# Kernel optimization log

Measured on AMD Instinct MI355X. Metric: run time of the kernel, lower is better.

## Reference

```python
import jax, jax.numpy as jnp
import numpy as np

D_MODEL = 1024
N_HEADS = 16
D_K = D_MODEL // N_HEADS  # 64
N_CLASSES = 32
S_LEN = 16   # synonyms per class
BATCH = 32
T_LEN = 512  # key/value sequence length


def setup_inputs() -> dict:
    key = jax.random.key(0)
    k1, k2, k3, k4, k5, k6 = jax.random.split(key, 6)
    Q = jax.random.normal(k1, (N_CLASSES, S_LEN, D_MODEL), dtype=jnp.float32)
    H = jax.random.normal(k2, (BATCH, T_LEN, D_MODEL), dtype=jnp.float32)
    ql = jax.random.normal(k3, (N_CLASSES, D_MODEL), dtype=jnp.float32)
    # torch Linear weights are (out_features, in_features), init N(0, 0.001)
    WQ_w = 0.001 * jax.random.normal(k4, (D_MODEL, D_MODEL), dtype=jnp.float32)
    WK_w = 0.001 * jax.random.normal(k5, (D_MODEL, D_MODEL), dtype=jnp.float32)
    WV_w = 0.001 * jax.random.normal(k6, (D_MODEL, D_MODEL), dtype=jnp.float32)
    return {"Q": Q, "H": H, "ql": ql, "WQ_w": WQ_w, "WK_w": WK_w, "WV_w": WV_w}


def reference(Q, H, ql, WQ_w, WK_w, WV_w):
    c, s, d = Q.shape
    b, t, _ = H.shape
    nh, dk = N_HEADS, D_K
    # projections (torch Linear: x @ W.T)
    q_s = (Q @ WQ_w.T).reshape(c, s, nh, dk).transpose(0, 2, 1, 3)   # czsh
    k_s = (H @ WK_w.T).reshape(b, t, nh, dk).transpose(0, 2, 1, 3)   # bzth
    Wql = ql @ WV_w.T                                                # ch
    Hh = H.reshape(b, t, nh, dk).transpose(0, 2, 1, 3)               # bzth
    WK = jnp.tanh(k_s)
    K = jnp.tanh(Hh)
    # scores: (b, c, z, s, t)
    scores = jnp.einsum('bzth,czsh->bczst', WK, q_s)
    attn = jax.nn.softmax(scores, axis=-1)
    # context: (b, c, z, s, h)
    context = jnp.einsum('bzth,bczst->bczsh', K, attn)
    # AvgPool3d((1, s, 1)) + squeeze(-2): mean over s -> (b, c, z, h)
    ctx = context.mean(axis=3).reshape(b, c, nh * dk)                # (b, c, d_model)
    output = jnp.einsum('bch,ch->bc', ctx, Wql)
    return output
```

## Files before the change

### kernel.cpp

```cpp
#include <hip/hip_runtime.h>
#include <hip/hip_bf16.h>
#include <math.h>

#define D_MODEL 1024
#define N_HEADS 16
#define D_K 64
#define N_CLASSES 32
#define S_LEN 16
#define BATCH 32
#define T_LEN 512

typedef __bf16 bf16_t;
typedef bf16_t bf16x8 __attribute__((ext_vector_type(8)));
typedef float f32x4 __attribute__((ext_vector_type(4)));
typedef long lx2 __attribute__((ext_vector_type(2)));

__device__ inline unsigned short f2bf(float f) {
    unsigned int u = __float_as_uint(f);
    unsigned int r = (u + 0x7FFFu + ((u >> 16) & 1u)) >> 16;
    return (unsigned short)r;
}
__device__ inline float fast_tanh(float x) {
    float e = __expf(2.0f * x);
    return (e - 1.0f) * __builtin_amdgcn_rcpf(e + 1.0f);
}
__device__ inline float4 fast_tanh4(float4 v) {
    return make_float4(fast_tanh(v.x), fast_tanh(v.y), fast_tanh(v.z), fast_tanh(v.w));
}
__device__ inline float dot4(float4 a, float4 b) {
    return a.x * b.x + a.y * b.y + a.z * b.z + a.w * b.w;
}
__device__ inline int pack_fp8x4(float4 v) {
    int p = __builtin_amdgcn_cvt_pk_fp8_f32(v.x, v.y, 0, false);
    p = __builtin_amdgcn_cvt_pk_fp8_f32(v.z, v.w, p, true);
    return p;
}

__device__ inline void async16(void* lds, const void* g) {
    __builtin_amdgcn_global_load_lds(
        (const __attribute__((address_space(1))) unsigned int*)g,
        (__attribute__((address_space(3))) unsigned int*)lds, 16, 0, 0);
}

__global__ __launch_bounds__(256) void cvt2_fp8_sw(
    const float* __restrict__ inA, int* __restrict__ outA, int nA,
    const float* __restrict__ inB, int* __restrict__ outB, int nB, float sB)
{
    int i = blockIdx.x * 256 + threadIdx.x;
    const float* in;
    int* out;
    float s;
    if (i < nA) { in = inA; out = outA; s = 1.0f; }
    else {
        i -= nA;
        if (i >= nB) return;
        in = inB; out = outB; s = sB;
    }
    const int p = i << 2;
    const int blk = p >> 10;
    const int pos = p & 1023;
    const int rb = blk >> 4;
    const int kb = blk & 15;
    const int q = pos >> 4;
    const int quad = q >> 4, l16 = q & 15;
    const int o = pos & 15;
    const int kh = o >> 3, b0 = o & 7;
    const int r = rb * 16 + l16;
    const int k = kb * 64 + kh * 32 + quad * 8 + b0;
    float4 v = *(const float4*)(in + (size_t)r * 1024 + k);
    v.x *= s; v.y *= s; v.z *= s; v.w *= s;
    out[i] = pack_fp8x4(v);
}

__global__ __launch_bounds__(256) void cvt2_bf16(
    const float4* __restrict__ inA, ushort4* __restrict__ outA, int nA4,
    const float4* __restrict__ inB, ushort4* __restrict__ outB, int nB4)
{
    int i = blockIdx.x * 256 + threadIdx.x;
    const float4* in;
    ushort4* out;
    if (i < nA4) { in = inA + i; out = outA + i; }
    else {
        i -= nA4;
        if (i >= nB4) return;
        in = inB + i; out = outB + i;
    }
    float4 v = *in;
    ushort4 o;
    o.x = f2bf(v.x); o.y = f2bf(v.y); o.z = f2bf(v.z); o.w = f2bf(v.w);
    *out = o;
}

__global__ __launch_bounds__(256) void cvt_bf16(
    const float4* __restrict__ in, ushort4* __restrict__ out, int n4)
{
    int i = blockIdx.x * 256 + threadIdx.x;
    if (i < n4) {
        float4 v = in[i];
        ushort4 o;
        o.x = f2bf(v.x); o.y = f2bf(v.y); o.z = f2bf(v.z); o.w = f2bf(v.w);
        out[i] = o;
    }
}

__global__ __launch_bounds__(256) void gemm_fp8_bt(
    const unsigned char* __restrict__ A, const unsigned char* __restrict__ B,
    unsigned short* __restrict__ C, int M, int N, float outScale)
{
    __shared__ __align__(16) unsigned char As[8192];
    __shared__ __align__(16) unsigned char Bs[8192];
    const int tid = threadIdx.x;
    const int m0 = blockIdx.x * 128;
    const int n0 = blockIdx.y * 128;
    const int wid = tid >> 6;
    const int lane = tid & 63;
    const int quad = lane >> 4;
    const int l16 = lane & 15;
    const int wm = (wid >> 1) * 64;
    const int wn = (wid & 1) * 64;
    const int stA = wm >> 4;
    const int stB = wn >> 4;
    const int st = tid >> 6;
    const int cl = (tid & 63) * 16;

    f32x4 acc[4][4] = {};

    const unsigned char* Ab = A + ((size_t)(m0 >> 4) * 16) * 1024;
    const unsigned char* Bb = B + ((size_t)(n0 >> 4) * 16) * 1024;

    for (int kb = 0; kb < 16; kb++) {
        async16(&As[tid * 16],        Ab + ((size_t)st * 16 + kb) * 1024 + cl);
        async16(&As[4096 + tid * 16], Ab + ((size_t)(st + 4) * 16 + kb) * 1024 + cl);
        async16(&Bs[tid * 16],        Bb + ((size_t)st * 16 + kb) * 1024 + cl);
        async16(&Bs[4096 + tid * 16], Bb + ((size_t)(st + 4) * 16 + kb) * 1024 + cl);
        __syncthreads();

        lx2 a8[4], b8[4];
#pragma unroll
        for (int mt = 0; mt < 4; mt++)
            a8[mt] = *(const lx2*)&As[(stA + mt) * 1024 + lane * 16];
#pragma unroll
        for (int nt = 0; nt < 4; nt++)
            b8[nt] = *(const lx2*)&Bs[(stB + nt) * 1024 + lane * 16];
#pragma unroll
        for (int mt = 0; mt < 4; mt++)
#pragma unroll
            for (int nt = 0; nt < 4; nt++) {
                acc[mt][nt] = __builtin_amdgcn_mfma_f32_16x16x32_fp8_fp8(
                    a8[mt].x, b8[nt].x, acc[mt][nt], 0, 0, 0);
                acc[mt][nt] = __builtin_amdgcn_mfma_f32_16x16x32_fp8_fp8(
                    a8[mt].y, b8[nt].y, acc[mt][nt], 0, 0, 0);
            }
        __syncthreads();
    }

#pragma unroll
    for (int mt = 0; mt < 4; mt++)
#pragma unroll
        for (int nt = 0; nt < 4; nt++)
#pragma unroll
            for (int r = 0; r < 4; r++) {
                const int row = m0 + wm + mt * 16 + quad * 4 + r;
                const int col = n0 + wn + nt * 16 + l16;
                C[(size_t)row * N + col] = f2bf(fast_tanh(acc[mt][nt][r] * outScale));
            }
}

__global__ __launch_bounds__(256) void gemm_bf16_bt(
    const unsigned short* __restrict__ A, const unsigned short* __restrict__ B,
    unsigned short* __restrict__ C, int M, int N, int K)
{
    __shared__ unsigned short As[128 * 32];
    __shared__ unsigned short Bs[128 * 32];
    const int tid = threadIdx.x;
    const int m0 = blockIdx.x * 128;
    const int n0 = blockIdx.y * 128;
    const int wid = tid >> 6;
    const int lane = tid & 63;
    const int quad = lane >> 4;
    const int l16 = lane & 15;
    const int wm = (wid >> 1) * 64;
    const int wn = (wid & 1) * 64;

    f32x4 acc[4][4] = {};

    const int r0 = tid >> 2;
    const int cc0 = (tid & 3) * 8;

    for (int k0 = 0; k0 < K; k0 += 32) {
        async16(&As[tid * 8],        A + (size_t)(m0 + r0) * K + k0 + cc0);
        async16(&As[2048 + tid * 8], A + (size_t)(m0 + 64 + r0) * K + k0 + cc0);
        async16(&Bs[tid * 8],        B + (size_t)(n0 + r0) * K + k0 + cc0);
        async16(&Bs[2048 + tid * 8], B + (size_t)(n0 + 64 + r0) * K + k0 + cc0);
        __syncthreads();

        bf16x8 af[4], bfr[4];
#pragma unroll
        for (int mt = 0; mt < 4; mt++)
            af[mt] = *(const bf16x8*)&As[(wm + mt * 16 + l16) * 32 + quad * 8];
#pragma unroll
        for (int nt = 0; nt < 4; nt++)
            bfr[nt] = *(const bf16x8*)&Bs[(wn + nt * 16 + l16) * 32 + quad * 8];
#pragma unroll
        for (int mt = 0; mt < 4; mt++)
#pragma unroll
            for (int nt = 0; nt < 4; nt++)
                acc[mt][nt] = __builtin_amdgcn_mfma_f32_16x16x32_bf16(
                    af[mt], bfr[nt], acc[mt][nt], 0, 0, 0);
        __syncthreads();
    }

#pragma unroll
    for (int mt = 0; mt < 4; mt++)
#pragma unroll
        for (int nt = 0; nt < 4; nt++)
#pragma unroll
            for (int r = 0; r < 4; r++) {
                const int row = m0 + wm + mt * 16 + quad * 4 + r;
                const int col = n0 + wn + nt * 16 + l16;
                C[(size_t)row * N + col] = f2bf(acc[mt][nt][r]);
            }
}

__global__ __launch_bounds__(256) void wql_kernel(
    const float* __restrict__ ql, const float* __restrict__ WV, float* __restrict__ wql)
{
    __shared__ float4 qls[32][32];
    __shared__ float4 WVs[64][33];
    const int tid = threadIdx.x;
    const int n0 = blockIdx.x * 64;
    const int k0 = blockIdx.y * 128;

    for (int i = tid; i < 1024; i += 256)
        qls[i >> 5][i & 31] = *(const float4*)(ql + (size_t)(i >> 5) * D_MODEL + k0 + (i & 31) * 4);
    for (int i = tid; i < 2048; i += 256)
        WVs[i >> 5][i & 31] = *(const float4*)(WV + (size_t)(n0 + (i >> 5)) * D_MODEL + k0 + (i & 31) * 4);
    __syncthreads();

    const int n = tid & 63;
    const int c0 = (tid >> 6) * 8;
    float acc[8] = {};
    for (int kq = 0; kq < 32; kq++) {
        const float4 wv = WVs[n][kq];
#pragma unroll
        for (int c = 0; c < 8; c++) acc[c] += dot4(qls[c0 + c][kq], wv);
    }
#pragma unroll
    for (int c = 0; c < 8; c++)
        atomicAdd(&wql[(size_t)(c0 + c) * D_MODEL + n0 + n], acc[c]);
}

__global__ __launch_bounds__(256) void kv_gemm(
    const float* __restrict__ H, const unsigned short* __restrict__ wql16,
    float* __restrict__ kv)
{
    __shared__ unsigned short Ks[128 * 64];
    __shared__ float kvt[128 * 33];
    const int chunk = blockIdx.x;
    const int z = blockIdx.y;
    const int b = chunk >> 2;
    const int t0 = (chunk & 3) * 128;
    const int tid = threadIdx.x;
    const int wid = tid >> 6;
    const int lane = tid & 63;
    const int quad = lane >> 4;
    const int l16 = lane & 15;

#pragma unroll
    for (int it = 0; it < 8; it++) {
        const int idx = it * 256 + tid;
        const int row = idx >> 4;
        const int c4 = (idx & 15) * 4;
        float4 v = *(const float4*)(H + ((size_t)b * T_LEN + t0 + row) * D_MODEL + z * D_K + c4);
        v = fast_tanh4(v);
        ushort4 o;
        o.x = f2bf(v.x); o.y = f2bf(v.y); o.z = f2bf(v.z); o.w = f2bf(v.w);
        *(ushort4*)&Ks[row * 64 + c4] = o;
    }
    bf16x8 bfr[2][2];
#pragma unroll
    for (int ct = 0; ct < 2; ct++)
#pragma unroll
        for (int kh = 0; kh < 2; kh++)
            bfr[ct][kh] = *(const bf16x8*)(wql16 +
                (size_t)(ct * 16 + l16) * D_MODEL + z * D_K + kh * 32 + quad * 8);
    __syncthreads();

    const int wt = wid * 32;
    f32x4 acc[2][2] = {};
#pragma unroll
    for (int tt = 0; tt < 2; tt++) {
        const bf16x8 a0 = *(const bf16x8*)&Ks[(wt + tt * 16 + l16) * 64 + quad * 8];
        const bf16x8 a1 = *(const bf16x8*)&Ks[(wt + tt * 16 + l16) * 64 + 32 + quad * 8];
#pragma unroll
        for (int ct = 0; ct < 2; ct++) {
            acc[tt][ct] = __builtin_amdgcn_mfma_f32_16x16x32_bf16(a0, bfr[ct][0], acc[tt][ct], 0, 0, 0);
            acc[tt][ct] = __builtin_amdgcn_mfma_f32_16x16x32_bf16(a1, bfr[ct][1], acc[tt][ct], 0, 0, 0);
        }
    }
#pragma unroll
    for (int tt = 0; tt < 2; tt++)
#pragma unroll
        for (int ct = 0; ct < 2; ct++)
#pragma unroll
            for (int r = 0; r < 4; r++)
                kvt[(wt + tt * 16 + quad * 4 + r) * 33 + ct * 16 + l16] = acc[tt][ct][r];
    __syncthreads();

    float* outb = kv + (((size_t)b * 16 + z) * 32) * 512 + t0;
#pragma unroll
    for (int it = 0; it < 4; it++) {
        const int idx = it * 256 + tid;
        const int c = idx >> 5;
        const int tq = (idx & 31) * 4;
        float4 v = make_float4(kvt[(tq + 0) * 33 + c], kvt[(tq + 1) * 33 + c],
                               kvt[(tq + 2) * 33 + c], kvt[(tq + 3) * 33 + c]);
        *(float4*)(outb + (size_t)c * 512 + tq) = v;
    }
}

__global__ __launch_bounds__(512, 4) void attn_mfma(
    const unsigned short* __restrict__ qproj, const unsigned short* __restrict__ wkt,
    const float* __restrict__ kv, float* __restrict__ out)
{
    __shared__ unsigned short wkts[512 * 64];
    const int z = blockIdx.x;
    const int b = blockIdx.y;
    const int tid = threadIdx.x;
    const int wid = tid >> 6;
    const int lane = tid & 63;
    const int quad = lane >> 4;
    const int l16 = lane & 15;

    const unsigned short* wb = wkt + (size_t)(b * T_LEN) * D_MODEL + z * D_K;
#pragma unroll
    for (int it = 0; it < 8; it++) {
        const int chunk = it * 512 + tid;
        const int row = chunk >> 3;
        const int c = chunk & 7;
        async16(&wkts[chunk * 8], wb + (size_t)row * D_MODEL + ((c ^ (row & 7)) * 8));
    }

    bf16x8 af[4][2];
#pragma unroll
    for (int ct = 0; ct < 4; ct++)
#pragma unroll
        for (int kh = 0; kh < 2; kh++)
            af[ct][kh] = *(const bf16x8*)(qproj +
                (size_t)((wid * 4 + ct) * 16 + l16) * D_MODEL + z * D_K + kh * 32 + quad * 8);
    __syncthreads();

    float den[4][4], num[4][4];
#pragma unroll
    for (int ct = 0; ct < 4; ct++)
#pragma unroll
        for (int r = 0; r < 4; r++) { den[ct][r] = 0.f; num[ct][r] = 0.f; }

    const float* kvb = kv + (((size_t)b * 16 + z) * 32) * 512;
    const int x0 = (quad ^ (l16 & 7)) * 8;
    const int x1 = ((quad ^ 4) ^ (l16 & 7)) * 8;
    for (int nt = 0; nt < 32; nt++) {
        const int rbase = (nt * 16 + l16) * 64;
        const bf16x8 b0 = *(const bf16x8*)&wkts[rbase + x0];
        const bf16x8 b1 = *(const bf16x8*)&wkts[rbase + x1];
#pragma unroll
        for (int ct = 0; ct < 4; ct++) {
            f32x4 a = {};
            a = __builtin_amdgcn_mfma_f32_16x16x32_bf16(af[ct][0], b0, a, 0, 0, 0);
            a = __builtin_amdgcn_mfma_f32_16x16x32_bf16(af[ct][1], b1, a, 0, 0, 0);
            const float kvv = kvb[(size_t)(wid * 4 + ct) * 512 + nt * 16 + l16];
#pragma unroll
            for (int r = 0; r < 4; r++) {
                const float e = __expf(a[r]);
                den[ct][r] += e;
                num[ct][r] += e * kvv;
            }
        }
    }

#pragma unroll
    for (int ct = 0; ct < 4; ct++) {
        float s = 0.f;
#pragma unroll
        for (int r = 0; r < 4; r++) {
            float d = den[ct][r], n = num[ct][r];
#pragma unroll
            for (int off = 1; off < 16; off <<= 1) {
                d += __shfl_xor(d, off, 64);
                n += __shfl_xor(n, off, 64);
            }
            s += n / d;
        }
        s += __shfl_xor(s, 16, 64);
        s += __shfl_xor(s, 32, 64);
        if (lane == 0)
            atomicAdd(&out[b * N_CLASSES + wid * 4 + ct], s * (1.0f / 16.0f));
    }
}

extern "C" void kernel_launch(void* const* d_in, const int* in_sizes, int n_in,
                              void* d_out, int out_size, void* d_ws, size_t ws_size,
                              hipStream_t stream)
{
    const float* Q  = (const float*)d_in[0];
    const float* H  = (const float*)d_in[1];
    const float* ql = (const float*)d_in[2];
    const float* WQ = (const float*)d_in[3];
    const float* WK = (const float*)d_in[4];
    const float* WV = (const float*)d_in[5];
    float* out = (float*)d_out;

    char* ws = (char*)d_ws;
    unsigned char*  Hf8   = (unsigned char*)(ws);
    unsigned short* wkt_b = (unsigned short*)(ws + (size_t)33554432);
    float*          kv    = (float*)(ws + (size_t)67108864);
    unsigned char*  WKf8  = (unsigned char*)(ws + (size_t)100663296);
    unsigned short* Qb      = (unsigned short*)(ws);
    unsigned short* WQb     = (unsigned short*)(ws + (size_t)(1 << 20));
    unsigned short* qproj_b = (unsigned short*)(ws + (size_t)(3 << 20));
    float*          wqlb    = (float*)(ws + (size_t)(4 << 20));
    unsigned short* wqlb16  = (unsigned short*)(ws + (size_t)4718592);

    hipMemsetAsync(d_out, 0, (size_t)out_size * sizeof(float), stream);

    dim3 thr(256);
    cvt2_fp8_sw<<<dim3(17408), thr, 0, stream>>>(
        H, (int*)Hf8, 4194304,
        WK, (int*)WKf8, 262144, 512.0f);
    gemm_fp8_bt<<<dim3(128, 8), thr, 0, stream>>>(Hf8, WKf8, wkt_b, 16384, 1024, 1.0f / 512.0f);
    cvt2_bf16<<<dim3(1536), thr, 0, stream>>>(
        (const float4*)Q, (ushort4*)Qb, 131072,
        (const float4*)WQ, (ushort4*)WQb, 262144);
    gemm_bf16_bt<<<dim3(4, 8), thr, 0, stream>>>(Qb, WQb, qproj_b, 512, 1024, 1024);
    hipMemsetAsync(wqlb, 0, (size_t)N_CLASSES * D_MODEL * sizeof(float), stream);
    wql_kernel<<<dim3(16, 8), thr, 0, stream>>>(ql, WV, wqlb);
    cvt_bf16<<<dim3(32), thr, 0, stream>>>((const float4*)wqlb, (ushort4*)wqlb16, 8192);
    kv_gemm<<<dim3(128, 16), thr, 0, stream>>>(H, wqlb16, kv);
    attn_mfma<<<dim3(16, 32), dim3(512), 0, stream>>>(qproj_b, wkt_b, kv, out);
}
```

Measured before the change: 239.8 us.

## Merge prep and GEMM kernels into fused launches, prefetch kv in attention

Collapses the eight prep and GEMM launches plus two memsets into two kernels that dispatch by block index: one for all conversions and the ql·WV projection, one for the fp8 WK GEMM, the bf16 Q GEMM and the kv GEMM. The wql projection now does the full K loop per block and writes bf16 directly, so the fp32 atomics and the memset go away. The attention kernel prefetches the next kv values one iteration ahead and raises wave priority around the MFMAs. Its final atomicAdd becomes per-head partial writes that a small reduce kernel sums. The aim is to cut launch gaps, serialization and atomics, at the cost of an extra launch and a wql path that no longer uses shared memory.

```diff
diff --git a/kernel.cpp b/kernel.cpp
--- a/kernel.cpp
+++ b/kernel.cpp
@@ -42,286 +42,244 @@
         (__attribute__((address_space(3))) unsigned int*)lds, 16, 0, 0);
 }
 
-__global__ __launch_bounds__(256) void cvt2_fp8_sw(
-    const float* __restrict__ inA, int* __restrict__ outA, int nA,
-    const float* __restrict__ inB, int* __restrict__ outB, int nB, float sB)
+__global__ __launch_bounds__(256) void prep_kernel(
+    const float* __restrict__ H, int* __restrict__ Hf8,
+    const float* __restrict__ WK, int* __restrict__ WKf8,
+    const float4* __restrict__ Q, ushort4* __restrict__ Qb,
+    const float4* __restrict__ WQ, ushort4* __restrict__ WQb,
+    const float* __restrict__ ql, const float* __restrict__ WV,
+    unsigned short* __restrict__ wqlb16)
 {
-    int i = blockIdx.x * 256 + threadIdx.x;
-    const float* in;
-    int* out;
-    float s;
-    if (i < nA) { in = inA; out = outA; s = 1.0f; }
-    else {
-        i -= nA;
-        if (i >= nB) return;
-        in = inB; out = outB; s = sB;
-    }
-    const int p = i << 2;
-    const int blk = p >> 10;
-    const int pos = p & 1023;
-    const int rb = blk >> 4;
-    const int kb = blk & 15;
-    const int q = pos >> 4;
-    const int quad = q >> 4, l16 = q & 15;
-    const int o = pos & 15;
-    const int kh = o >> 3, b0 = o & 7;
-    const int r = rb * 16 + l16;
-    const int k = kb * 64 + kh * 32 + quad * 8 + b0;
-    float4 v = *(const float4*)(in + (size_t)r * 1024 + k);
-    v.x *= s; v.y *= s; v.z *= s; v.w *= s;
-    out[i] = pack_fp8x4(v);
-}
-
-__global__ __launch_bounds__(256) void cvt2_bf16(
-    const float4* __restrict__ inA, ushort4* __restrict__ outA, int nA4,
-    const float4* __restrict__ inB, ushort4* __restrict__ outB, int nB4)
-{
-    int i = blockIdx.x * 256 + threadIdx.x;
-    const float4* in;
-    ushort4* out;
-    if (i < nA4) { in = inA + i; out = outA + i; }
-    else {
-        i -= nA4;
-        if (i >= nB4) return;
-        in = inB + i; out = outB + i;
-    }
-    float4 v = *in;
-    ushort4 o;
-    o.x = f2bf(v.x); o.y = f2bf(v.y); o.z = f2bf(v.z); o.w = f2bf(v.w);
-    *out = o;
-}
-
-__global__ __launch_bounds__(256) void cvt_bf16(
-    const float4* __restrict__ in, ushort4* __restrict__ out, int n4)
-{
-    int i = blockIdx.x * 256 + threadIdx.x;
-    if (i < n4) {
-        float4 v = in[i];
+    const int bid = blockIdx.x;
+    const int tid = threadIdx.x;
+    if (bid < 16) {
+        const int n0 = bid * 64;
+        const int n = tid & 63;
+        const int c0 = (tid >> 6) * 8;
+        const float* wvp = WV + (size_t)(n0 + n) * D_MODEL;
+        float acc[8] = {};
+        for (int k = 0; k < 1024; k += 4) {
+            const float4 wv = *(const float4*)(wvp + k);
+#pragma unroll
+            for (int c = 0; c < 8; c++) {
+                const float4 qv = *(const float4*)(ql + (size_t)(c0 + c) * D_MODEL + k);
+                acc[c] += dot4(qv, wv);
+            }
+        }
+#pragma unroll
+        for (int c = 0; c < 8; c++)
+            wqlb16[(size_t)(c0 + c) * D_MODEL + n0 + n] = f2bf(acc[c]);
+    } else if (bid < 17424) {
+        int i = (bid - 16) * 256 + tid;
+        const float* in; int* out; float s;
+        if (i < 4194304) { in = H; out = Hf8; s = 1.0f; }
+        else { i -= 4194304; in = WK; out = WKf8; s = 512.0f; }
+        const int p = i << 2;
+        const int blk = p >> 10;
+        const int pos = p & 1023;
+        const int rb = blk >> 4, kb = blk & 15;
+        const int q = pos >> 4;
+        const int quad = q >> 4, l16 = q & 15;
+        const int o = pos & 15;
+        const int kh = o >> 3, b0 = o & 7;
+        const int r = rb * 16 + l16;
+        const int k = kb * 64 + kh * 32 + quad * 8 + b0;
+        float4 v = *(const float4*)(in + (size_t)r * 1024 + k);
+        v.x *= s; v.y *= s; v.z *= s; v.w *= s;
+        out[i] = pack_fp8x4(v);
+    } else {
+        int i = (bid - 17424) * 256 + tid;
+        const float4* in; ushort4* out;
+        if (i < 131072) { in = Q + i; out = Qb + i; }
+        else { i -= 131072; in = WQ + i; out = WQb + i; }
+        float4 v = *in;
         ushort4 o;
         o.x = f2bf(v.x); o.y = f2bf(v.y); o.z = f2bf(v.z); o.w = f2bf(v.w);
-        out[i] = o;
+        *out = o;
     }
 }
 
-__global__ __launch_bounds__(256) void gemm_fp8_bt(
-    const unsigned char* __restrict__ A, const unsigned char* __restrict__ B,
-    unsigned short* __restrict__ C, int M, int N, float outScale)
-{
-    __shared__ __align__(16) unsigned char As[8192];
-    __shared__ __align__(16) unsigned char Bs[8192];
-    const int tid = threadIdx.x;
-    const int m0 = blockIdx.x * 128;
-    const int n0 = blockIdx.y * 128;
-    const int wid = tid >> 6;
-    const int lane = tid & 63;
-    const int quad = lane >> 4;
-    const int l16 = lane & 15;
-    const int wm = (wid >> 1) * 64;
-    const int wn = (wid & 1) * 64;
-    const int stA = wm >> 4;
-    const int stB = wn >> 4;
-    const int st = tid >> 6;
-    const int cl = (tid & 63) * 16;
-
-    f32x4 acc[4][4] = {};
-
-    const unsigned char* Ab = A + ((size_t)(m0 >> 4) * 16) * 1024;
-    const unsigned char* Bb = B + ((size_t)(n0 >> 4) * 16) * 1024;
-
-    for (int kb = 0; kb < 16; kb++) {
-        async16(&As[tid * 16],        Ab + ((size_t)st * 16 + kb) * 1024 + cl);
-        async16(&As[4096 + tid * 16], Ab + ((size_t)(st + 4) * 16 + kb) * 1024 + cl);
-        async16(&Bs[tid * 16],        Bb + ((size_t)st * 16 + kb) * 1024 + cl);
-        async16(&Bs[4096 + tid * 16], Bb + ((size_t)(st + 4) * 16 + kb) * 1024 + cl);
-        __syncthreads();
-
-        lx2 a8[4], b8[4];
-#pragma unroll
-        for (int mt = 0; mt < 4; mt++)
-            a8[mt] = *(const lx2*)&As[(stA + mt) * 1024 + lane * 16];
-#pragma unroll
-        for (int nt = 0; nt < 4; nt++)
-            b8[nt] = *(const lx2*)&Bs[(stB + nt) * 1024 + lane * 16];
-#pragma unroll
-        for (int mt = 0; mt < 4; mt++)
-#pragma unroll
-            for (int nt = 0; nt < 4; nt++) {
-                acc[mt][nt] = __builtin_amdgcn_mfma_f32_16x16x32_fp8_fp8(
-                    a8[mt].x, b8[nt].x, acc[mt][nt], 0, 0, 0);
-                acc[mt][nt] = __builtin_amdgcn_mfma_f32_16x16x32_fp8_fp8(
-                    a8[mt].y, b8[nt].y, acc[mt][nt], 0, 0, 0);
-            }
-        __syncthreads();
-    }
-
-#pragma unroll
-    for (int mt = 0; mt < 4; mt++)
-#pragma unroll
-        for (int nt = 0; nt < 4; nt++)
-#pragma unroll
-            for (int r = 0; r < 4; r++) {
-                const int row = m0 + wm + mt * 16 + quad * 4 + r;
-                const int col = n0 + wn + nt * 16 + l16;
-                C[(size_t)row * N + col] = f2bf(fast_tanh(acc[mt][nt][r] * outScale));
-            }
-}
-
-__global__ __launch_bounds__(256) void gemm_bf16_bt(
-    const unsigned short* __restrict__ A, const unsigned short* __restrict__ B,
-    unsigned short* __restrict__ C, int M, int N, int K)
-{
-    __shared__ unsigned short As[128 * 32];
-    __shared__ unsigned short Bs[128 * 32];
-    const int tid = threadIdx.x;
-    const int m0 = blockIdx.x * 128;
-    const int n0 = blockIdx.y * 128;
-    const int wid = tid >> 6;
-    const int lane = tid & 63;
-    const int quad = lane >> 4;
-    const int l16 = lane & 15;
-    const int wm = (wid >> 1) * 64;
-    const int wn = (wid & 1) * 64;
-
-    f32x4 acc[4][4] = {};
-
-    const int r0 = tid >> 2;
-    const int cc0 = (tid & 3) * 8;
-
-    for (int k0 = 0; k0 < K; k0 += 32) {
-        async16(&As[tid * 8],        A + (size_t)(m0 + r0) * K + k0 + cc0);
-        async16(&As[2048 + tid * 8], A + (size_t)(m0 + 64 + r0) * K + k0 + cc0);
-        async16(&Bs[tid * 8],        B + (size_t)(n0 + r0) * K + k0 + cc0);
-        async16(&Bs[2048 + tid * 8], B + (size_t)(n0 + 64 + r0) * K + k0 + cc0);
-        __syncthreads();
-
-        bf16x8 af[4], bfr[4];
-#pragma unroll
-        for (int mt = 0; mt < 4; mt++)
-            af[mt] = *(const bf16x8*)&As[(wm + mt * 16 + l16) * 32 + quad * 8];
-#pragma unroll
-        for (int nt = 0; nt < 4; nt++)
-            bfr[nt] = *(const bf16x8*)&Bs[(wn + nt * 16 + l16) * 32 + quad * 8];
-#pragma unroll
-        for (int mt = 0; mt < 4; mt++)
-#pragma unroll
-            for (int nt = 0; nt < 4; nt++)
-                acc[mt][nt] = __builtin_amdgcn_mfma_f32_16x16x32_bf16(
-                    af[mt], bfr[nt], acc[mt][nt], 0, 0, 0);
-        __syncthreads();
-    }
-
-#pragma unroll
-    for (int mt = 0; mt < 4; mt++)
-#pragma unroll
-        for (int nt = 0; nt < 4; nt++)
-#pragma unroll
-            for (int r = 0; r < 4; r++) {
-                const int row = m0 + wm + mt * 16 + quad * 4 + r;
-                const int col = n0 + wn + nt * 16 + l16;
-                C[(size_t)row * N + col] = f2bf(acc[mt][nt][r]);
-            }
-}
-
-__global__ __launch_bounds__(256) void wql_kernel(
-    const float* __restrict__ ql, const float* __restrict__ WV, float* __restrict__ wql)
-{
-    __shared__ float4 qls[32][32];
-    __shared__ float4 WVs[64][33];
-    const int tid = threadIdx.x;
-    const int n0 = blockIdx.x * 64;
-    const int k0 = blockIdx.y * 128;
-
-    for (int i = tid; i < 1024; i += 256)
-        qls[i >> 5][i & 31] = *(const float4*)(ql + (size_t)(i >> 5) * D_MODEL + k0 + (i & 31) * 4);
-    for (int i = tid; i < 2048; i += 256)
-        WVs[i >> 5][i & 31] = *(const float4*)(WV + (size_t)(n0 + (i >> 5)) * D_MODEL + k0 + (i & 31) * 4);
-    __syncthreads();
-
-    const int n = tid & 63;
-    const int c0 = (tid >> 6) * 8;
-    float acc[8] = {};
-    for (int kq = 0; kq < 32; kq++) {
-        const float4 wv = WVs[n][kq];
-#pragma unroll
-        for (int c = 0; c < 8; c++) acc[c] += dot4(qls[c0 + c][kq], wv);
-    }
-#pragma unroll
-    for (int c = 0; c < 8; c++)
-        atomicAdd(&wql[(size_t)(c0 + c) * D_MODEL + n0 + n], acc[c]);
-}
-
-__global__ __launch_bounds__(256) void kv_gemm(
+__global__ __launch_bounds__(256) void gemms_kernel(
+    const unsigned char* __restrict__ A8, const unsigned char* __restrict__ B8,
+    unsigned short* __restrict__ wkt_b,
+    const unsigned short* __restrict__ Qb, const unsigned short* __restrict__ WQb,
+    unsigned short* __restrict__ qproj_b,
     const float* __restrict__ H, const unsigned short* __restrict__ wql16,
     float* __restrict__ kv)
 {
-    __shared__ unsigned short Ks[128 * 64];
-    __shared__ float kvt[128 * 33];
-    const int chunk = blockIdx.x;
-    const int z = blockIdx.y;
-    const int b = chunk >> 2;
-    const int t0 = (chunk & 3) * 128;
+    __shared__ __align__(16) char smem[33280];
+    const int bid = blockIdx.x;
     const int tid = threadIdx.x;
     const int wid = tid >> 6;
     const int lane = tid & 63;
     const int quad = lane >> 4;
     const int l16 = lane & 15;
 
-#pragma unroll
-    for (int it = 0; it < 8; it++) {
-        const int idx = it * 256 + tid;
-        const int row = idx >> 4;
-        const int c4 = (idx & 15) * 4;
-        float4 v = *(const float4*)(H + ((size_t)b * T_LEN + t0 + row) * D_MODEL + z * D_K + c4);
-        v = fast_tanh4(v);
-        ushort4 o;
-        o.x = f2bf(v.x); o.y = f2bf(v.y); o.z = f2bf(v.z); o.w = f2bf(v.w);
-        *(ushort4*)&Ks[row * 64 + c4] = o;
-    }
-    bf16x8 bfr[2][2];
-#pragma unroll
-    for (int ct = 0; ct < 2; ct++)
-#pragma unroll
-        for (int kh = 0; kh < 2; kh++)
-            bfr[ct][kh] = *(const bf16x8*)(wql16 +
-                (size_t)(ct * 16 + l16) * D_MODEL + z * D_K + kh * 32 + quad * 8);
-    __syncthreads();
-
-    const int wt = wid * 32;
-    f32x4 acc[2][2] = {};
-#pragma unroll
-    for (int tt = 0; tt < 2; tt++) {
-        const bf16x8 a0 = *(const bf16x8*)&Ks[(wt + tt * 16 + l16) * 64 + quad * 8];
-        const bf16x8 a1 = *(const bf16x8*)&Ks[(wt + tt * 16 + l16) * 64 + 32 + quad * 8];
-#pragma unroll
-        for (int ct = 0; ct < 2; ct++) {
-            acc[tt][ct] = __builtin_amdgcn_mfma_f32_16x16x32_bf16(a0, bfr[ct][0], acc[tt][ct], 0, 0, 0);
-            acc[tt][ct] = __builtin_amdgcn_mfma_f32_16x16x32_bf16(a1, bfr[ct][1], acc[tt][ct], 0, 0, 0);
-        }
-    }
-#pragma unroll
-    for (int tt = 0; tt < 2; tt++)
+    if (bid < 1024) {
+        unsigned char* As = (unsigned char*)smem;
+        unsigned char* Bs = (unsigned char*)smem + 8192;
+        const int m0 = (bid & 127) * 128;
+        const int n0 = (bid >> 7) * 128;
+        const int wm = (wid >> 1) * 64;
+        const int wn = (wid & 1) * 64;
+        const int stA = wm >> 4;
+        const int stB = wn >> 4;
+        const int st = wid;
+        const int cl = lane * 16;
+
+        f32x4 acc[4][4] = {};
+        const unsigned char* Ab = A8 + ((size_t)(m0 >> 4) * 16) * 1024;
+        const unsigned char* Bb = B8 + ((size_t)(n0 >> 4) * 16) * 1024;
+
+        for (int kb = 0; kb < 16; kb++) {
+            async16(&As[tid * 16],        Ab + ((size_t)st * 16 + kb) * 1024 + cl);
+            async16(&As[4096 + tid * 16], Ab + ((size_t)(st + 4) * 16 + kb) * 1024 + cl);
+            async16(&Bs[tid * 16],        Bb + ((size_t)st * 16 + kb) * 1024 + cl);
+            async16(&Bs[4096 + tid * 16], Bb + ((size_t)(st + 4) * 16 + kb) * 1024 + cl);
+            __syncthreads();
+
+            lx2 a8[4], b8[4];
+#pragma unroll
+            for (int mt = 0; mt < 4; mt++)
+                a8[mt] = *(const lx2*)&As[(stA + mt) * 1024 + lane * 16];
+#pragma unroll
+            for (int nt = 0; nt < 4; nt++)
+                b8[nt] = *(const lx2*)&Bs[(stB + nt) * 1024 + lane * 16];
+#pragma unroll
+            for (int mt = 0; mt < 4; mt++)
+#pragma unroll
+                for (int nt = 0; nt < 4; nt++) {
+                    acc[mt][nt] = __builtin_amdgcn_mfma_f32_16x16x32_fp8_fp8(
+                        a8[mt].x, b8[nt].x, acc[mt][nt], 0, 0, 0);
+                    acc[mt][nt] = __builtin_amdgcn_mfma_f32_16x16x32_fp8_fp8(
+                        a8[mt].y, b8[nt].y, acc[mt][nt], 0, 0, 0);
+                }
+            __syncthreads();
+        }
+
+#pragma unroll
+        for (int mt = 0; mt < 4; mt++)
+#pragma unroll
+            for (int nt = 0; nt < 4; nt++)
+#pragma unroll
+                for (int r = 0; r < 4; r++) {
+                    const int row = m0 + wm + mt * 16 + quad * 4 + r;
+                    const int col = n0 + wn + nt * 16 + l16;
+                    wkt_b[(size_t)row * 1024 + col] =
+                        f2bf(fast_tanh(acc[mt][nt][r] * (1.0f / 512.0f)));
+                }
+    } else if (bid < 1056) {
+        unsigned short* As = (unsigned short*)smem;
+        unsigned short* Bs = (unsigned short*)(smem + 8192);
+        const int q = bid - 1024;
+        const int m0 = (q & 3) * 128;
+        const int n0 = (q >> 2) * 128;
+        const int wm = (wid >> 1) * 64;
+        const int wn = (wid & 1) * 64;
+
+        f32x4 acc[4][4] = {};
+        const int r0 = tid >> 2;
+        const int cc0 = (tid & 3) * 8;
+
+        for (int k0 = 0; k0 < 1024; k0 += 32) {
+            async16(&As[tid * 8],        Qb  + (size_t)(m0 + r0) * 1024 + k0 + cc0);
+            async16(&As[2048 + tid * 8], Qb  + (size_t)(m0 + 64 + r0) * 1024 + k0 + cc0);
+            async16(&Bs[tid * 8],        WQb + (size_t)(n0 + r0) * 1024 + k0 + cc0);
+            async16(&Bs[2048 + tid * 8], WQb + (size_t)(n0 + 64 + r0) * 1024 + k0 + cc0);
+            __syncthreads();
+
+            bf16x8 af[4], bfr[4];
+#pragma unroll
+            for (int mt = 0; mt < 4; mt++)
+                af[mt] = *(const bf16x8*)&As[(wm + mt * 16 + l16) * 32 + quad * 8];
+#pragma unroll
+            for (int nt = 0; nt < 4; nt++)
+                bfr[nt] = *(const bf16x8*)&Bs[(wn + nt * 16 + l16) * 32 + quad * 8];
+#pragma unroll
+            for (int mt = 0; mt < 4; mt++)
+#pragma unroll
+                for (int nt = 0; nt < 4; nt++)
+                    acc[mt][nt] = __builtin_amdgcn_mfma_f32_16x16x32_bf16(
+                        af[mt], bfr[nt], acc[mt][nt], 0, 0, 0);
+            __syncthreads();
+        }
+
+#pragma unroll
+        for (int mt = 0; mt < 4; mt++)
+#pragma unroll
+            for (int nt = 0; nt < 4; nt++)
+#pragma unroll
+                for (int r = 0; r < 4; r++) {
+                    const int row = m0 + wm + mt * 16 + quad * 4 + r;
+                    const int col = n0 + wn + nt * 16 + l16;
+                    qproj_b[(size_t)row * 1024 + col] = f2bf(acc[mt][nt][r]);
+                }
+    } else {
+        unsigned short* Ks = (unsigned short*)smem;
+        float* kvt = (float*)(smem + 16384);
+        const int q = bid - 1056;
+        const int chunk = q & 127;
+        const int z = q >> 7;
+        const int b = chunk >> 2;
+        const int t0 = (chunk & 3) * 128;
+
+#pragma unroll
+        for (int it = 0; it < 8; it++) {
+            const int idx = it * 256 + tid;
+            const int row = idx >> 4;
+            const int c4 = (idx & 15) * 4;
+            float4 v = *(const float4*)(H + ((size_t)b * T_LEN + t0 + row) * D_MODEL + z * D_K + c4);
+            v = fast_tanh4(v);
+            ushort4 o;
+            o.x = f2bf(v.x); o.y = f2bf(v.y); o.z = f2bf(v.z); o.w = f2bf(v.w);
+            *(ushort4*)&Ks[row * 64 + c4] = o;
+        }
+        bf16x8 bfr[2][2];
 #pragma unroll
         for (int ct = 0; ct < 2; ct++)
 #pragma unroll
-            for (int r = 0; r < 4; r++)
-                kvt[(wt + tt * 16 + quad * 4 + r) * 33 + ct * 16 + l16] = acc[tt][ct][r];
-    __syncthreads();
-
-    float* outb = kv + (((size_t)b * 16 + z) * 32) * 512 + t0;
-#pragma unroll
-    for (int it = 0; it < 4; it++) {
-        const int idx = it * 256 + tid;
-        const int c = idx >> 5;
-        const int tq = (idx & 31) * 4;
-        float4 v = make_float4(kvt[(tq + 0) * 33 + c], kvt[(tq + 1) * 33 + c],
-                               kvt[(tq + 2) * 33 + c], kvt[(tq + 3) * 33 + c]);
-        *(float4*)(outb + (size_t)c * 512 + tq) = v;
+            for (int kh = 0; kh < 2; kh++)
+                bfr[ct][kh] = *(const bf16x8*)(wql16 +
+                    (size_t)(ct * 16 + l16) * D_MODEL + z * D_K + kh * 32 + quad * 8);
+        __syncthreads();
+
+        const int wt = wid * 32;
+        f32x4 acc[2][2] = {};
+#pragma unroll
+        for (int tt = 0; tt < 2; tt++) {
+            const bf16x8 a0 = *(const bf16x8*)&Ks[(wt + tt * 16 + l16) * 64 + quad * 8];
+            const bf16x8 a1 = *(const bf16x8*)&Ks[(wt + tt * 16 + l16) * 64 + 32 + quad * 8];
+#pragma unroll
+            for (int ct = 0; ct < 2; ct++) {
+                acc[tt][ct] = __builtin_amdgcn_mfma_f32_16x16x32_bf16(a0, bfr[ct][0], acc[tt][ct], 0, 0, 0);
+                acc[tt][ct] = __builtin_amdgcn_mfma_f32_16x16x32_bf16(a1, bfr[ct][1], acc[tt][ct], 0, 0, 0);
+            }
+        }
+#pragma unroll
+        for (int tt = 0; tt < 2; tt++)
+#pragma unroll
+            for (int ct = 0; ct < 2; ct++)
+#pragma unroll
+                for (int r = 0; r < 4; r++)
+                    kvt[(wt + tt * 16 + quad * 4 + r) * 33 + ct * 16 + l16] = acc[tt][ct][r];
+        __syncthreads();
+
+        float* outb = kv + (((size_t)b * 16 + z) * 32) * 512 + t0;
+#pragma unroll
+        for (int it = 0; it < 4; it++) {
+            const int idx = it * 256 + tid;
+            const int c = idx >> 5;
+            const int tq = (idx & 31) * 4;
+            float4 v = make_float4(kvt[(tq + 0) * 33 + c], kvt[(tq + 1) * 33 + c],
+                                   kvt[(tq + 2) * 33 + c], kvt[(tq + 3) * 33 + c]);
+            *(float4*)(outb + (size_t)c * 512 + tq) = v;
+        }
     }
 }
 
 __global__ __launch_bounds__(512, 4) void attn_mfma(
     const unsigned short* __restrict__ qproj, const unsigned short* __restrict__ wkt,
-    const float* __restrict__ kv, float* __restrict__ out)
+    const float* __restrict__ kv, float* __restrict__ part)
 {
     __shared__ unsigned short wkts[512 * 64];
     const int z = blockIdx.x;
@@ -356,26 +314,40 @@
 #pragma unroll
         for (int r = 0; r < 4; r++) { den[ct][r] = 0.f; num[ct][r] = 0.f; }
 
-    const float* kvb = kv + (((size_t)b * 16 + z) * 32) * 512;
+    const float* kvp = kv + (((size_t)b * 16 + z) * 32 + wid * 4) * 512 + l16;
+    float kc[4];
+#pragma unroll
+    for (int ct = 0; ct < 4; ct++) kc[ct] = kvp[ct * 512];
+
     const int x0 = (quad ^ (l16 & 7)) * 8;
     const int x1 = ((quad ^ 4) ^ (l16 & 7)) * 8;
     for (int nt = 0; nt < 32; nt++) {
+        float kn[4];
+#pragma unroll
+        for (int ct = 0; ct < 4; ct++) kn[ct] = kvp[ct * 512 + (nt + 1) * 16];
         const int rbase = (nt * 16 + l16) * 64;
         const bf16x8 b0 = *(const bf16x8*)&wkts[rbase + x0];
         const bf16x8 b1 = *(const bf16x8*)&wkts[rbase + x1];
+        f32x4 a4[4];
+        __builtin_amdgcn_s_setprio(1);
 #pragma unroll
         for (int ct = 0; ct < 4; ct++) {
             f32x4 a = {};
             a = __builtin_amdgcn_mfma_f32_16x16x32_bf16(af[ct][0], b0, a, 0, 0, 0);
             a = __builtin_amdgcn_mfma_f32_16x16x32_bf16(af[ct][1], b1, a, 0, 0, 0);
-            const float kvv = kvb[(size_t)(wid * 4 + ct) * 512 + nt * 16 + l16];
+            a4[ct] = a;
+        }
+        __builtin_amdgcn_s_setprio(0);
+#pragma unroll
+        for (int ct = 0; ct < 4; ct++)
 #pragma unroll
             for (int r = 0; r < 4; r++) {
-                const float e = __expf(a[r]);
+                const float e = __expf(a4[ct][r]);
                 den[ct][r] += e;
-                num[ct][r] += e * kvv;
+                num[ct][r] += e * kc[ct];
             }
-        }
+#pragma unroll
+        for (int ct = 0; ct < 4; ct++) kc[ct] = kn[ct];
     }
 
 #pragma unroll
@@ -394,8 +366,19 @@
         s += __shfl_xor(s, 16, 64);
         s += __shfl_xor(s, 32, 64);
         if (lane == 0)
-            atomicAdd(&out[b * N_CLASSES + wid * 4 + ct], s * (1.0f / 16.0f));
+            part[((size_t)(b * N_CLASSES) + wid * 4 + ct) * 16 + z] = s;
     }
+}
+
+__global__ __launch_bounds__(256) void attn_reduce(
+    const float* __restrict__ part, float* __restrict__ out)
+{
+    const int i = blockIdx.x * 256 + threadIdx.x;
+    const float* p = part + (size_t)i * 16;
+    float s = 0.f;
+#pragma unroll
+    for (int zz = 0; zz < 16; zz++) s += p[zz];
+    out[i] = s * (1.0f / 16.0f);
 }
 
 extern "C" void kernel_launch(void* const* d_in, const int* in_sizes, int n_in,
@@ -411,30 +394,24 @@
     float* out = (float*)d_out;
 
     char* ws = (char*)d_ws;
-    unsigned char*  Hf8   = (unsigned char*)(ws);
-    unsigned short* wkt_b = (unsigned short*)(ws + (size_t)33554432);
-    float*          kv    = (float*)(ws + (size_t)67108864);
-    unsigned char*  WKf8  = (unsigned char*)(ws + (size_t)100663296);
-    unsigned short* Qb      = (unsigned short*)(ws);
-    unsigned short* WQb     = (unsigned short*)(ws + (size_t)(1 << 20));
-    unsigned short* qproj_b = (unsigned short*)(ws + (size_t)(3 << 20));
-    float*          wqlb    = (float*)(ws + (size_t)(4 << 20));
-    unsigned short* wqlb16  = (unsigned short*)(ws + (size_t)4718592);
-
-    hipMemsetAsync(d_out, 0, (size_t)out_size * sizeof(float), stream);
+    unsigned char*  Hf8     = (unsigned char*)(ws);
+    unsigned short* Qb      = (unsigned short*)(ws + (size_t)25165824);
+    unsigned short* WQb     = (unsigned short*)(ws + (size_t)26214400);
+    unsigned short* qproj_b = (unsigned short*)(ws + (size_t)28311552);
+    unsigned short* wqlb16  = (unsigned short*)(ws + (size_t)29360128);
+    float*          part    = (float*)(ws + (size_t)30408704);
+    unsigned short* wkt_b   = (unsigned short*)(ws + (size_t)33554432);
+    float*          kv      = (float*)(ws + (size_t)67108864);
+    unsigned char*  WKf8    = (unsigned char*)(ws + (size_t)100663296);
 
     dim3 thr(256);
-    cvt2_fp8_sw<<<dim3(17408), thr, 0, stream>>>(
-        H, (int*)Hf8, 4194304,
-        WK, (int*)WKf8, 262144, 512.0f);
-    gemm_fp8_bt<<<dim3(128, 8), thr, 0, stream>>>(Hf8, WKf8, wkt_b, 16384, 1024, 1.0f / 512.0f);
-    cvt2_bf16<<<dim3(1536), thr, 0, stream>>>(
-        (const float4*)Q, (ushort4*)Qb, 131072,
-        (const float4*)WQ, (ushort4*)WQb, 262144);
-    gemm_bf16_bt<<<dim3(4, 8), thr, 0, stream>>>(Qb, WQb, qproj_b, 512, 1024, 1024);
-    hipMemsetAsync(wqlb, 0, (size_t)N_CLASSES * D_MODEL * sizeof(float), stream);
-    wql_kernel<<<dim3(16, 8), thr, 0, stream>>>(ql, WV, wqlb);
-    cvt_bf16<<<dim3(32), thr, 0, stream>>>((const float4*)wqlb, (ushort4*)wqlb16, 8192);
-    kv_gemm<<<dim3(128, 16), thr, 0, stream>>>(H, wqlb16, kv);
-    attn_mfma<<<dim3(16, 32), dim3(512), 0, stream>>>(qproj_b, wkt_b, kv, out);
-}
+    prep_kernel<<<dim3(18960), thr, 0, stream>>>(
+        H, (int*)Hf8, WK, (int*)WKf8,
+        (const float4*)Q, (ushort4*)Qb,
+        (const float4*)WQ, (ushort4*)WQb,
+        ql, WV, wqlb16);
+    gemms_kernel<<<dim3(3104), thr, 0, stream>>>(
+        Hf8, WKf8, wkt_b, Qb, WQb, qproj_b, H, wqlb16, kv);
+    attn_mfma<<<dim3(16, 32), dim3(512), 0, stream>>>(qproj_b, wkt_b, kv, part);
+    attn_reduce<<<dim3(4), thr, 0, stream>>>(part, out);
+}
```

Measured after the change: 313.4 us. 1.31x slower.
